# Kernel optimization log

Hardware: AMD Instinct MI355X
Metric: run time of the kernel (lower is better)

The kernel has to match this reference:

```python
import jax, jax.numpy as jnp
import numpy as np

M, N, P, T = 8000, 63, 64, 5


def setup_inputs() -> dict:
    key = jax.random.key(0)
    ks = jax.random.split(key, 19)
    sn = (1.0 / N) ** 0.5
    sp = (1.0 / P) ** 0.5
    f32 = jnp.float32
    return {
        "A": jax.random.normal(ks[0], (1, M, N), f32),
        "b": jax.random.normal(ks[1], (1, M), f32),
        "c": jax.random.normal(ks[2], (1, N), f32),
        "theta1r": sn * jax.random.normal(ks[3], (P, N + 1), f32),
        "theta1c": sn * jax.random.normal(ks[4], (P, N + 1), f32),
        "theta2rr": sp * jax.random.normal(ks[5], (P, P), f32),
        "theta2rc": sp * jax.random.normal(ks[6], (P, P), f32),
        "theta2cr": sp * jax.random.normal(ks[7], (P, P), f32),
        "theta3rr": sp * jax.random.normal(ks[8], (P, P), f32),
        "theta3rc": sp * jax.random.normal(ks[9], (P, P), f32),
        "theta3cr": sp * jax.random.normal(ks[10], (P, P), f32),
        "theta4rr": sp * jax.random.normal(ks[11], (P,), f32),
        "theta4rc": sp * jax.random.normal(ks[12], (P,), f32),
        "theta4cr": sp * jax.random.normal(ks[13], (P,), f32),
        "theta6r": sp * jax.random.normal(ks[14], (P, P), f32),
        "theta6c": sp * jax.random.normal(ks[15], (P, P), f32),
        "theta7": sp * jax.random.normal(ks[16], (P, P), f32),
        "W8": 0.05 * jax.random.normal(ks[17], (2, 2 * P), f32),
        "b8": 0.05 * jax.random.normal(ks[18], (2,), f32),
        "z": 7,
    }


def reference(A, b, c, theta1r, theta1c, theta2rr, theta2rc, theta2cr,
              theta3rr, theta3rc, theta3cr, theta4rr, theta4rc, theta4cr,
              theta6r, theta6c, theta7, W8, b8, z):
    relu = jax.nn.relu
    m, n = A.shape[1], A.shape[2]
    p = theta1r.shape[0]
    # raw node features: row node v -> [A[v,:], b[v]]; column node m -> [c, 0]
    Fr_raw = jnp.concatenate([A[0], b[0][:, None]], axis=1)        # (m, n+1)
    fc_raw = jnp.concatenate([c[0], jnp.zeros((1,), A.dtype)])     # (n+1,)
    Fr = Fr_raw / jnp.linalg.norm(Fr_raw, axis=1, keepdims=True)   # f(v), v < m
    fc = fc_raw / jnp.linalg.norm(fc_raw)                          # f(m)
    # edge weights w(v,u) = f(v).f(u) are detached in the original (float(...data))
    Frd = jax.lax.stop_gradient(Fr)
    fcd = jax.lax.stop_gradient(fc)
    Wrr = Frd @ Frd.T                                              # (m, m)
    dg = jnp.diagonal(Wrr)
    srr_pos = relu(Wrr).sum(axis=1) - relu(dg)                     # sum over u != v
    srr_neg = relu(-Wrr).sum(axis=1) - relu(-dg)
    wrc = Frd @ fcd                                                # (m,) = w(v, m)
    # identity: sum_u relu(t4 * w_u) = relu(t4) * sum_u relu(w_u) + relu(-t4) * sum_u relu(-w_u)
    Srr = relu(theta4rr)[:, None] * srr_pos[None, :] + relu(-theta4rr)[:, None] * srr_neg[None, :]
    Src = relu(theta4rc)[:, None] * relu(wrc)[None, :] + relu(-theta4rc)[:, None] * relu(-wrc)[None, :]
    scr = relu(theta4cr) * relu(wrc).sum() + relu(-theta4cr) * relu(-wrc).sum()
    edge_r = theta3rr @ Srr + theta3rc @ Src                       # (p, m), constant over t
    edge_c = theta3cr @ scr                                        # (p,)
    fz = Fr[z]                                                     # z < m: row node feature
    t1r = theta1r @ fz                                             # (p,)
    t1c = theta1c @ fz
    # mu init (p, m+1) = [[Ab^T, c0^T]; 0]; split into row columns / column node
    mu_r0 = jnp.zeros((p, m), A.dtype).at[: n + 1].set(Fr_raw.T)
    mu_c0 = jnp.zeros((p,), A.dtype).at[: n + 1].set(fc_raw)

    def step(carry, _):
        mu_r, mu_c = carry
        # row nodes: term2rr uses old mu[:, v]; term2rc uses old mu[:, m]
        new_r = relu(t1r[:, None] + theta2rr @ mu_r + (theta2rc @ mu_c)[:, None] + edge_r)
        # column node updated last within a sweep -> sees updated row embeddings
        new_c = relu(t1c + theta2cr @ new_r.sum(axis=1) + edge_c)
        return (new_r, new_c), None

    (mu_r, mu_c), _ = jax.lax.scan(step, (mu_r0, mu_c0), None, length=T)
    term6 = theta6r @ mu_r.sum(axis=1) + theta6c @ mu_c            # (p,)
    term7 = theta7 @ mu_r[:, z]                                    # (p,)
    feat = jax.nn.sigmoid(jnp.concatenate([term6, term7]))         # (2p,)
    return (feat @ W8.T + b8)[None, :]                             # (1, 2)
```

## Files before the change

kernel.cpp:

```cpp
#include <hip/hip_runtime.h>
#include <math.h>

typedef __attribute__((ext_vector_type(8))) short short8;
typedef __attribute__((ext_vector_type(4))) float f32x4;

#define WS_SPART 0
#define WS_GPART 131072
#define WS_WPART 163840
#define WS_CPART 164864
#define WS_T1R   204864
#define WS_T1C   204928
#define WS_AL    204992
#define WS_BE    205056
#define WS_GA    205120
#define WS_DE    205184
#define WS_ECP   205248
#define WS_ECN   205312
#define WS_W     205376
#define WS_MUZ   205760
#define WS_WSUM  205824
#define WS_RNORM 205888
#define WS_R2H   214080
#define WS_R2L   216128
#define WS_E4    218176
#define WS_FH    250176
#define WS_FL    512320

__device__ __forceinline__ float waveReduceSum(float v) {
#pragma unroll
    for (int m = 32; m >= 1; m >>= 1) v += __shfl_xor(v, m, 64);
    return v;
}
__device__ __forceinline__ unsigned short f2bf(float f) {
    unsigned int u = __float_as_uint(f);
    unsigned int r = (u + 0x7fffu + ((u >> 16) & 1u)) >> 16;
    return (unsigned short)r;
}
__device__ __forceinline__ float bf2f(unsigned short h) {
    return __uint_as_float(((unsigned int)h) << 16);
}

__global__ __launch_bounds__(256) void k_fr(
    const float* __restrict__ A, const float* __restrict__ b, const float* __restrict__ c,
    const float* __restrict__ th1r, const float* __restrict__ th1c,
    const float* __restrict__ th2rr, const float* __restrict__ th2rc,
    const float* __restrict__ th3rr, const float* __restrict__ th3rc, const float* __restrict__ th3cr,
    const float* __restrict__ th4rr, const float* __restrict__ th4rc, const float* __restrict__ th4cr,
    const int* __restrict__ zp,
    unsigned short* __restrict__ Fh, unsigned short* __restrict__ Fl,
    unsigned short* __restrict__ R2H, unsigned short* __restrict__ R2L,
    float* __restrict__ ws)
{
    int tid = threadIdx.x, lane = tid & 63, wid = tid >> 6;

    if (blockIdx.x == 512) {
        __shared__ float fcraw[64], fz[64], sh4a[64], sh4b[64];
        int p = lane;
        int z = zp[0];
        float cv = (p < 63) ? c[p] : 0.f;
        fcraw[p] = cv;
        float av = (p < 63) ? A[z * 63 + p] : b[z];
        float s2 = waveReduceSum(av * av);
        fz[p] = av * rsqrtf(s2);
        __syncthreads();

        float t1 = 0.f, t2 = 0.f, w0 = 0.f;
#pragma unroll 8
        for (int k = 0; k < 64; k++) {
            t1 += th1r[p * 64 + k] * fz[k];
            t2 += th1c[p * 64 + k] * fz[k];
            w0 += th2rc[p * 64 + k] * fcraw[k];
        }
        ws[WS_T1R + p] = t1;
        ws[WS_T1C + p] = t2;
        ws[WS_W + p] = t1 + w0;

        sh4a[p] = th4rr[p];
        sh4b[p] = th4rc[p];
        __syncthreads();
        float a = 0.f, bb = 0.f, g = 0.f, d = 0.f;
#pragma unroll 8
        for (int k = 0; k < 64; k++) {
            float t4 = sh4a[k];
            a  += th3rr[p * 64 + k] * fmaxf(t4, 0.f);
            bb += th3rr[p * 64 + k] * fmaxf(-t4, 0.f);
            float t5 = sh4b[k];
            g  += th3rc[p * 64 + k] * fmaxf(t5, 0.f);
            d  += th3rc[p * 64 + k] * fmaxf(-t5, 0.f);
        }
        ws[WS_AL + p] = a; ws[WS_BE + p] = bb;
        ws[WS_GA + p] = g; ws[WS_DE + p] = d;
        __syncthreads();
        sh4a[p] = th4cr[p];
        __syncthreads();
        float e1 = 0.f, e2 = 0.f;
#pragma unroll 8
        for (int k = 0; k < 64; k++) {
            float t6 = sh4a[k];
            e1 += th3cr[p * 64 + k] * fmaxf(t6, 0.f);
            e2 += th3cr[p * 64 + k] * fmaxf(-t6, 0.f);
        }
        ws[WS_ECP + p] = e1; ws[WS_ECN + p] = e2;

#pragma unroll
        for (int i = 0; i < 16; i++) {
            int idx = tid * 16 + i;
            float f = th2rr[idx];
            unsigned short h = f2bf(f);
            R2H[idx] = h;
            R2L[idx] = f2bf(f - bf2f(h));
        }
        return;
    }

    __shared__ float gsh[64];
    __shared__ float wsh2[2];
    if (tid < 64) gsh[tid] = 0.f;
    if (tid < 2) wsh2[tid] = 0.f;
    __syncthreads();

    float cv = (lane < 63) ? c[lane] : 0.f;
    float cn2 = waveReduceSum(cv * cv);
    float fcnl = cv * rsqrtf(cn2);

    int r0 = blockIdx.x * 16 + wid * 4;
    float gl = 0.f, lp = 0.f, ln = 0.f;
#pragma unroll
    for (int i = 0; i < 4; i++) {
        int r = r0 + i;
        if (r < 8000) {
            float val = (lane < 63) ? A[r * 63 + lane] : b[r];
            float s2 = waveReduceSum(val * val);
            float f = val * rsqrtf(s2);
            unsigned short h = f2bf(f);
            Fh[r * 64 + lane] = h;
            Fl[r * 64 + lane] = f2bf(f - bf2f(h));
            gl += f;
            float w = waveReduceSum(f * fcnl);
            if (lane == 0) {
                ws[WS_RNORM + r] = sqrtf(s2);
                lp += fmaxf(w, 0.f); ln += fmaxf(-w, 0.f);
            }
        } else {
            Fh[r * 64 + lane] = 0;
            Fl[r * 64 + lane] = 0;
        }
    }
    atomicAdd(&gsh[lane], gl);
    if (lane == 0) { atomicAdd(&wsh2[0], lp); atomicAdd(&wsh2[1], ln); }
    __syncthreads();
    if (tid < 64) ws[WS_GPART + blockIdx.x * 64 + tid] = gsh[tid];
    if (tid == 64) ws[WS_WPART + blockIdx.x * 2 + 0] = wsh2[0];
    if (tid == 65) ws[WS_WPART + blockIdx.x * 2 + 1] = wsh2[1];
}

__global__ __launch_bounds__(256) void k_gram(
    const unsigned short* __restrict__ Fh, float* __restrict__ ws)
{
    __shared__ short Bsh[2][32 * 72];
    int tid = threadIdx.x, lane = tid & 63, wid = tid >> 6;
    int m = lane & 15, quad = lane >> 4;
    int vbase = blockIdx.x * 256 + wid * 64;
    int srow = tid >> 3;
    int scol = (tid & 7) * 8;

    short8 AH[8];
#pragma unroll
    for (int pt = 0; pt < 4; pt++)
#pragma unroll
        for (int q = 0; q < 2; q++)
            AH[pt * 2 + q] = *(const short8*)(Fh + (vbase + pt * 16 + m) * 64 + q * 32 + quad * 8);

    float srr[16];
#pragma unroll
    for (int i = 0; i < 16; i++) srr[i] = 0.f;

    const int y = blockIdx.y;
    *(short8*)(&Bsh[0][srow * 72 + scol]) = *(const short8*)(Fh + (y * 32 + srow) * 64 + scol);
    __syncthreads();

#pragma unroll 1
    for (int k = 0; k < 16; k++) {
        int cur = k & 1;
        short8 pre;
        if (k < 15) {
            int cch = y + 16 * (k + 1);
            pre = *(const short8*)(Fh + (cch * 32 + srow) * 64 + scol);
        }
#pragma unroll
        for (int s = 0; s < 2; s++) {
            short8 BH[2];
#pragma unroll
            for (int q = 0; q < 2; q++)
                BH[q] = *(const short8*)(&Bsh[cur][(s * 16 + m) * 72 + q * 32 + quad * 8]);
#pragma unroll
            for (int pt = 0; pt < 4; pt++) {
                f32x4 a = {0.f, 0.f, 0.f, 0.f};
                a = __builtin_amdgcn_mfma_f32_16x16x32_bf16(AH[pt * 2 + 0], BH[0], a, 0, 0, 0);
                a = __builtin_amdgcn_mfma_f32_16x16x32_bf16(AH[pt * 2 + 1], BH[1], a, 0, 0, 0);
#pragma unroll
                for (int r = 0; r < 4; r++) srr[pt * 4 + r] += fmaxf(a[r], 0.f);
            }
        }
        if (k < 15) {
            *(short8*)(&Bsh[1 - cur][srow * 72 + scol]) = pre;
            __syncthreads();
        }
    }
#pragma unroll
    for (int pt = 0; pt < 4; pt++)
#pragma unroll
        for (int r = 0; r < 4; r++) {
            float s = srr[pt * 4 + r];
            s += __shfl_xor(s, 1, 64); s += __shfl_xor(s, 2, 64);
            s += __shfl_xor(s, 4, 64); s += __shfl_xor(s, 8, 64);
            if (m == 0)
                ws[WS_SPART + y * 8192 + vbase + pt * 16 + quad * 4 + r] = s;
        }
}

__global__ __launch_bounds__(256) void k_mu0(
    const float* __restrict__ c, float* __restrict__ ws,
    unsigned short* __restrict__ MH, unsigned short* __restrict__ ML,
    const unsigned short* __restrict__ R2H, const unsigned short* __restrict__ R2L)
{
    __shared__ float XF[64][68];
    __shared__ float red[256], colp[256];
    __shared__ __align__(16) float wS[64], alS[64], beS[64], gaS[64], deS[64];
    __shared__ float fcnS[64], gS[64], sprow[64];
    __shared__ __align__(16) float e4sh[256];
    int tid = threadIdx.x, lane = tid & 63, wid = tid >> 6;
    int m = lane & 15, quad = lane >> 4;
    int v0 = blockIdx.x * 64;
    int cw = wid * 16 + m;
    int v = v0 + cw;

    if (wid == 0) {
        float cv = (lane < 63) ? c[lane] : 0.f;
        float cn2 = waveReduceSum(cv * cv);
        fcnS[lane] = cv * rsqrtf(cn2);
        wS[lane] = ws[WS_W + lane];
    } else if (wid == 1) {
        alS[lane] = ws[WS_AL + lane]; beS[lane] = ws[WS_BE + lane];
        float wp = 0.f;
#pragma unroll
        for (int k = 0; k < 8; k++) wp += ws[WS_WPART + (lane + 64 * k) * 2];
        wp = waveReduceSum(wp);
        if (lane == 0) ws[WS_WSUM] = wp;
    } else if (wid == 2) {
        gaS[lane] = ws[WS_GA + lane]; deS[lane] = ws[WS_DE + lane];
        float wn = 0.f;
#pragma unroll
        for (int k = 0; k < 8; k++) wn += ws[WS_WPART + (lane + 64 * k) * 2 + 1];
        wn = waveReduceSum(wn);
        if (lane == 0) ws[WS_WSUM + 1] = wn;
    }
    float gv = 0.f;
#pragma unroll 8
    for (int bb = 0; bb < 128; bb++) gv += ws[WS_GPART + (wid * 128 + bb) * 64 + lane];
    red[tid] = gv;
    __syncthreads();
    if (tid < 64) gS[tid] = red[tid] + red[64 + tid] + red[128 + tid] + red[192 + tid];
    __syncthreads();
    float sv = 0.f;
#pragma unroll
    for (int y = wid * 4; y < wid * 4 + 4; y++) sv += ws[WS_SPART + y * 8192 + v0 + lane];
    red[tid] = sv;
    __syncthreads();
    if (tid < 64) sprow[tid] = red[tid] + red[64 + tid] + red[128 + tid] + red[192 + tid];
    __syncthreads();

    for (int i2 = 0; i2 < 16; i2++) {
        int i = wid * 16 + i2;
        int vr = v0 + i;
        float fr = bf2f(MH[vr * 64 + lane]) + bf2f(ML[vr * 64 + lane]);
        float dw = waveReduceSum(fr * fcnS[lane]);
        float dg = waveReduceSum(fr * gS[lane]);
        if (lane == 0) {
            float spv = sprow[i];
            float4 e;
            e.x = spv - 1.0f;
            e.y = spv - dg;
            e.z = fmaxf(dw, 0.f);
            e.w = fmaxf(-dw, 0.f);
            *(float4*)(&e4sh[i * 4]) = e;
            *(float4*)(ws + WS_E4 + vr * 4) = e;
        }
        XF[i][lane] = fr * ws[WS_RNORM + vr];
    }

    short8 RH[8], RL[8];
#pragma unroll
    for (int pt = 0; pt < 4; pt++)
#pragma unroll
        for (int q = 0; q < 2; q++) {
            int off = (pt * 16 + m) * 64 + q * 32 + quad * 8;
            RH[pt * 2 + q] = *(const short8*)(R2H + off);
            RL[pt * 2 + q] = *(const short8*)(R2L + off);
        }
    __syncthreads();

    short8 BH[2], BL[2];
#pragma unroll
    for (int q = 0; q < 2; q++) {
        float4 f0 = *(const float4*)(&XF[cw][q * 32 + quad * 8]);
        float4 f1 = *(const float4*)(&XF[cw][q * 32 + quad * 8 + 4]);
        float xv[8] = {f0.x, f0.y, f0.z, f0.w, f1.x, f1.y, f1.z, f1.w};
        short8 H, L;
#pragma unroll
        for (int j = 0; j < 8; j++) {
            unsigned short h = f2bf(xv[j]);
            H[j] = (short)h;
            L[j] = (short)f2bf(xv[j] - bf2f(h));
        }
        BH[q] = H; BL[q] = L;
    }
    float4 e = *(const float4*)(&e4sh[cw * 4]);

#pragma unroll
    for (int pt = 0; pt < 4; pt++) {
        f32x4 a = {0.f, 0.f, 0.f, 0.f};
#pragma unroll
        for (int q = 0; q < 2; q++) {
            a = __builtin_amdgcn_mfma_f32_16x16x32_bf16(RH[pt*2+q], BH[q], a, 0, 0, 0);
            a = __builtin_amdgcn_mfma_f32_16x16x32_bf16(RH[pt*2+q], BL[q], a, 0, 0, 0);
            a = __builtin_amdgcn_mfma_f32_16x16x32_bf16(RL[pt*2+q], BH[q], a, 0, 0, 0);
        }
        int pbase = pt * 16 + quad * 4;
        float4 w4 = *(const float4*)(wS + pbase);
        float4 a4 = *(const float4*)(alS + pbase);
        float4 b4 = *(const float4*)(beS + pbase);
        float4 g4 = *(const float4*)(gaS + pbase);
        float4 d4 = *(const float4*)(deS + pbase);
        float u0 = fmaxf(a[0] + w4.x + a4.x*e.x + b4.x*e.y + g4.x*e.z + d4.x*e.w, 0.f);
        float u1 = fmaxf(a[1] + w4.y + a4.y*e.x + b4.y*e.y + g4.y*e.z + d4.y*e.w, 0.f);
        float u2 = fmaxf(a[2] + w4.z + a4.z*e.x + b4.z*e.y + g4.z*e.z + d4.z*e.w, 0.f);
        float u3 = fmaxf(a[3] + w4.w + a4.w*e.x + b4.w*e.y + g4.w*e.z + d4.w*e.w, 0.f);
        ushort4 h4, l4;
        h4.x = f2bf(u0); l4.x = f2bf(u0 - bf2f(h4.x));
        h4.y = f2bf(u1); l4.y = f2bf(u1 - bf2f(h4.y));
        h4.z = f2bf(u2); l4.z = f2bf(u2 - bf2f(h4.z));
        h4.w = f2bf(u3); l4.w = f2bf(u3 - bf2f(h4.w));
        *(ushort4*)(MH + v * 64 + pbase) = h4;
        *(ushort4*)(ML + v * 64 + pbase) = l4;
        float c0 = u0, c1 = u1, c2 = u2, c3 = u3;
#pragma unroll
        for (int mm = 1; mm < 16; mm <<= 1) {
            c0 += __shfl_xor(c0, mm, 64);
            c1 += __shfl_xor(c1, mm, 64);
            c2 += __shfl_xor(c2, mm, 64);
            c3 += __shfl_xor(c3, mm, 64);
        }
        if (m == 0) {
            colp[wid * 64 + pbase + 0] = c0;
            colp[wid * 64 + pbase + 1] = c1;
            colp[wid * 64 + pbase + 2] = c2;
            colp[wid * 64 + pbase + 3] = c3;
        }
    }
    __syncthreads();
    if (tid < 64)
        ws[WS_CPART + blockIdx.x * 64 + tid] =
            colp[tid] + colp[64 + tid] + colp[128 + tid] + colp[192 + tid];
}

__global__ __launch_bounds__(256) void k_mu(
    const int* __restrict__ zp, float* __restrict__ ws,
    unsigned short* __restrict__ MH, unsigned short* __restrict__ ML,
    const unsigned short* __restrict__ R2H, const unsigned short* __restrict__ R2L,
    int t)
{
    __shared__ __align__(16) float wS[64], alS[64], beS[64], gaS[64], deS[64];
    __shared__ float colp[256];
    int tid = threadIdx.x, lane = tid & 63, wid = tid >> 6;
    int m = lane & 15, quad = lane >> 4;
    int v = (blockIdx.x * 4 + wid) * 16 + m;
    int z = zp[0];

    if (wid == 0) wS[lane] = ws[WS_W + t * 64 + lane];
    else if (wid == 1) { alS[lane] = ws[WS_AL + lane]; beS[lane] = ws[WS_BE + lane]; }
    else if (wid == 2) { gaS[lane] = ws[WS_GA + lane]; deS[lane] = ws[WS_DE + lane]; }

    short8 RH[8], RL[8];
#pragma unroll
    for (int pt = 0; pt < 4; pt++)
#pragma unroll
        for (int q = 0; q < 2; q++) {
            int off = (pt * 16 + m) * 64 + q * 32 + quad * 8;
            RH[pt * 2 + q] = *(const short8*)(R2H + off);
            RL[pt * 2 + q] = *(const short8*)(R2L + off);
        }
    short8 BH[2], BL[2];
#pragma unroll
    for (int q = 0; q < 2; q++) {
        BH[q] = *(const short8*)(MH + v * 64 + q * 32 + quad * 8);
        BL[q] = *(const short8*)(ML + v * 64 + q * 32 + quad * 8);
    }
    float4 e = *(const float4*)(ws + WS_E4 + v * 4);
    __syncthreads();

#pragma unroll
    for (int pt = 0; pt < 4; pt++) {
        f32x4 a = {0.f, 0.f, 0.f, 0.f};
#pragma unroll
        for (int q = 0; q < 2; q++) {
            a = __builtin_amdgcn_mfma_f32_16x16x32_bf16(RH[pt*2+q], BH[q], a, 0, 0, 0);
            a = __builtin_amdgcn_mfma_f32_16x16x32_bf16(RH[pt*2+q], BL[q], a, 0, 0, 0);
            a = __builtin_amdgcn_mfma_f32_16x16x32_bf16(RL[pt*2+q], BH[q], a, 0, 0, 0);
        }
        int pbase = pt * 16 + quad * 4;
        float4 w4 = *(const float4*)(wS + pbase);
        float4 a4 = *(const float4*)(alS + pbase);
        float4 b4 = *(const float4*)(beS + pbase);
        float4 g4 = *(const float4*)(gaS + pbase);
        float4 d4 = *(const float4*)(deS + pbase);
        float u0 = fmaxf(a[0] + w4.x + a4.x*e.x + b4.x*e.y + g4.x*e.z + d4.x*e.w, 0.f);
        float u1 = fmaxf(a[1] + w4.y + a4.y*e.x + b4.y*e.y + g4.y*e.z + d4.y*e.w, 0.f);
        float u2 = fmaxf(a[2] + w4.z + a4.z*e.x + b4.z*e.y + g4.z*e.z + d4.z*e.w, 0.f);
        float u3 = fmaxf(a[3] + w4.w + a4.w*e.x + b4.w*e.y + g4.w*e.z + d4.w*e.w, 0.f);
        ushort4 h4, l4;
        h4.x = f2bf(u0); l4.x = f2bf(u0 - bf2f(h4.x));
        h4.y = f2bf(u1); l4.y = f2bf(u1 - bf2f(h4.y));
        h4.z = f2bf(u2); l4.z = f2bf(u2 - bf2f(h4.z));
        h4.w = f2bf(u3); l4.w = f2bf(u3 - bf2f(h4.w));
        *(ushort4*)(MH + v * 64 + pbase) = h4;
        *(ushort4*)(ML + v * 64 + pbase) = l4;
        float c0 = u0, c1 = u1, c2 = u2, c3 = u3;
#pragma unroll
        for (int mm = 1; mm < 16; mm <<= 1) {
            c0 += __shfl_xor(c0, mm, 64);
            c1 += __shfl_xor(c1, mm, 64);
            c2 += __shfl_xor(c2, mm, 64);
            c3 += __shfl_xor(c3, mm, 64);
        }
        if (m == 0) {
            colp[wid * 64 + pbase + 0] = c0;
            colp[wid * 64 + pbase + 1] = c1;
            colp[wid * 64 + pbase + 2] = c2;
            colp[wid * 64 + pbase + 3] = c3;
        }
        if (t == 4 && v == z) {
            float4 o; o.x = u0; o.y = u1; o.z = u2; o.w = u3;
            *(float4*)(ws + WS_MUZ + pbase) = o;
        }
    }
    __syncthreads();
    if (tid < 64)
        ws[WS_CPART + t * 8000 + blockIdx.x * 64 + tid] =
            colp[tid] + colp[64 + tid] + colp[128 + tid] + colp[192 + tid];
}

__global__ __launch_bounds__(256) void k_colup(
    const float* __restrict__ th2cr, const float* __restrict__ th2rc,
    const float* __restrict__ th6r, const float* __restrict__ th6c,
    const float* __restrict__ th7, const float* __restrict__ W8,
    const float* __restrict__ b8,
    float* __restrict__ ws, float* __restrict__ out, int t)
{
    __shared__ float red[256], Ssh[64], ysh[64], wsh[64], feat[128];
    int tid = threadIdx.x, lane = tid & 63, wid = tid >> 6;
    int m = lane & 15, quad = lane >> 4;

    float s = 0.f;
    for (int blk = wid; blk < 125; blk += 4)
        s += ws[WS_CPART + t * 8000 + blk * 64 + lane];
    red[tid] = s;
    __syncthreads();
    if (tid < 64) Ssh[tid] = red[tid] + red[64 + tid] + red[128 + tid] + red[192 + tid];
    __syncthreads();
    {
        int p = wid * 16 + m;
        float acc = 0.f;
        const float4* rowp = (const float4*)(th2cr + p * 64 + quad * 16);
#pragma unroll
        for (int kk = 0; kk < 4; kk++) {
            float4 r4 = rowp[kk];
            acc += r4.x * Ssh[quad * 16 + 4 * kk]     + r4.y * Ssh[quad * 16 + 4 * kk + 1]
                 + r4.z * Ssh[quad * 16 + 4 * kk + 2] + r4.w * Ssh[quad * 16 + 4 * kk + 3];
        }
        acc += __shfl_xor(acc, 16, 64);
        acc += __shfl_xor(acc, 32, 64);
        if (quad == 0)
            ysh[p] = fmaxf(acc + ws[WS_T1C + p] + ws[WS_WSUM] * ws[WS_ECP + p]
                           + ws[WS_WSUM + 1] * ws[WS_ECN + p], 0.f);
    }
    __syncthreads();
    {
        int p = wid * 16 + m;
        float acc = 0.f;
        const float4* rowp = (const float4*)(th2rc + p * 64 + quad * 16);
#pragma unroll
        for (int kk = 0; kk < 4; kk++) {
            float4 r4 = rowp[kk];
            acc += r4.x * ysh[quad * 16 + 4 * kk]     + r4.y * ysh[quad * 16 + 4 * kk + 1]
                 + r4.z * ysh[quad * 16 + 4 * kk + 2] + r4.w * ysh[quad * 16 + 4 * kk + 3];
        }
        acc += __shfl_xor(acc, 16, 64);
        acc += __shfl_xor(acc, 32, 64);
        if (quad == 0) wsh[p] = acc + ws[WS_T1R + p];
    }
    __syncthreads();
    if (tid < 64) ws[WS_W + (t + 1) * 64 + tid] = wsh[tid];

    if (t == 4) {
        int p = tid;
        if (p < 64) {
            float t6 = 0.f, t7 = 0.f;
#pragma unroll 8
            for (int k = 0; k < 64; k++) {
                t6 += th6r[p * 64 + k] * Ssh[k] + th6c[p * 64 + k] * ysh[k];
                t7 += th7[p * 64 + k] * ws[WS_MUZ + k];
            }
            feat[p] = 1.f / (1.f + expf(-t6));
            feat[64 + p] = 1.f / (1.f + expf(-t7));
        }
        __syncthreads();
        if (p < 2) {
            float o = b8[p];
            for (int i = 0; i < 128; i++) o += W8[p * 128 + i] * feat[i];
            out[p] = o;
        }
    }
}

extern "C" void kernel_launch(void* const* d_in, const int* in_sizes, int n_in,
                              void* d_out, int out_size, void* d_ws, size_t ws_size,
                              hipStream_t stream) {
    (void)in_sizes; (void)n_in; (void)out_size; (void)ws_size;
    const float* A     = (const float*)d_in[0];
    const float* b     = (const float*)d_in[1];
    const float* c     = (const float*)d_in[2];
    const float* th1r  = (const float*)d_in[3];
    const float* th1c  = (const float*)d_in[4];
    const float* th2rr = (const float*)d_in[5];
    const float* th2rc = (const float*)d_in[6];
    const float* th2cr = (const float*)d_in[7];
    const float* th3rr = (const float*)d_in[8];
    const float* th3rc = (const float*)d_in[9];
    const float* th3cr = (const float*)d_in[10];
    const float* th4rr = (const float*)d_in[11];
    const float* th4rc = (const float*)d_in[12];
    const float* th4cr = (const float*)d_in[13];
    const float* th6r  = (const float*)d_in[14];
    const float* th6c  = (const float*)d_in[15];
    const float* th7   = (const float*)d_in[16];
    const float* W8    = (const float*)d_in[17];
    const float* b8    = (const float*)d_in[18];
    const int*   zp    = (const int*)d_in[19];
    float* ws  = (float*)d_ws;
    float* out = (float*)d_out;
    unsigned short* Fh  = (unsigned short*)(ws + WS_FH);
    unsigned short* Fl  = (unsigned short*)(ws + WS_FL);
    unsigned short* R2H = (unsigned short*)(ws + WS_R2H);
    unsigned short* R2L = (unsigned short*)(ws + WS_R2L);

    k_fr<<<513, 256, 0, stream>>>(A, b, c, th1r, th1c, th2rr, th2rc, th3rr, th3rc,
                                  th3cr, th4rr, th4rc, th4cr, zp, Fh, Fl, R2H, R2L, ws);
    k_gram<<<dim3(32, 16), 256, 0, stream>>>(Fh, ws);
    k_mu0<<<125, 256, 0, stream>>>(c, ws, Fh, Fl, R2H, R2L);
    for (int t = 0; t < 5; t++) {
        k_colup<<<1, 256, 0, stream>>>(th2cr, th2rc, th6r, th6c, th7, W8, b8, ws, out, t);
        if (t < 4)
            k_mu<<<125, 256, 0, stream>>>(zp, ws, Fh, Fl, R2H, R2L, t + 1);
    }
}
```

Measured before the change: 224.3 us.

## Fuse column-node update into k_mu and drop LDS staging in gram kernel

The single-block k_colup launches between iterations are removed. Every k_mu block now reduces the column partials itself and recomputes the column-node update and the row bias, and a separate k_head kernel computes the final output. This removes four serial one-block launches at the cost of redundant small matvecs in each of the 125 blocks. The gram kernel also stops staging B tiles in LDS and loads 16-row tiles straight into registers with a two-stage register prefetch. Its grid is doubled in y, so the partial-sum workspace and its reduction grow to match.

Result: no change. 223.9 us (-0.2%).

```diff
diff --git a/kernel.cpp b/kernel.cpp
--- a/kernel.cpp
+++ b/kernel.cpp
@@ -5,26 +5,26 @@
 typedef __attribute__((ext_vector_type(4))) float f32x4;
 
 #define WS_SPART 0
-#define WS_GPART 131072
-#define WS_WPART 163840
-#define WS_CPART 164864
-#define WS_T1R   204864
-#define WS_T1C   204928
-#define WS_AL    204992
-#define WS_BE    205056
-#define WS_GA    205120
-#define WS_DE    205184
-#define WS_ECP   205248
-#define WS_ECN   205312
-#define WS_W     205376
-#define WS_MUZ   205760
-#define WS_WSUM  205824
-#define WS_RNORM 205888
-#define WS_R2H   214080
-#define WS_R2L   216128
-#define WS_E4    218176
-#define WS_FH    250176
-#define WS_FL    512320
+#define WS_GPART 262144
+#define WS_WPART 294912
+#define WS_CPART 295936
+#define WS_T1R   335936
+#define WS_T1C   336000
+#define WS_AL    336064
+#define WS_BE    336128
+#define WS_GA    336192
+#define WS_DE    336256
+#define WS_ECP   336320
+#define WS_ECN   336384
+#define WS_W     336448
+#define WS_MUZ   336512
+#define WS_WSUM  336576
+#define WS_RNORM 336640
+#define WS_R2H   344832
+#define WS_R2L   346880
+#define WS_E4    348928
+#define WS_FH    380928
+#define WS_FL    643072
 
 __device__ __forceinline__ float waveReduceSum(float v) {
 #pragma unroll
@@ -157,12 +157,9 @@
 __global__ __launch_bounds__(256) void k_gram(
     const unsigned short* __restrict__ Fh, float* __restrict__ ws)
 {
-    __shared__ short Bsh[2][32 * 72];
     int tid = threadIdx.x, lane = tid & 63, wid = tid >> 6;
     int m = lane & 15, quad = lane >> 4;
     int vbase = blockIdx.x * 256 + wid * 64;
-    int srow = tid >> 3;
-    int scol = (tid & 7) * 8;
 
     short8 AH[8];
 #pragma unroll
@@ -176,35 +173,39 @@
     for (int i = 0; i < 16; i++) srr[i] = 0.f;
 
     const int y = blockIdx.y;
-    *(short8*)(&Bsh[0][srow * 72 + scol]) = *(const short8*)(Fh + (y * 32 + srow) * 64 + scol);
-    __syncthreads();
+    const int boff = m * 64 + quad * 8;
+    short8 B0[2], B1[2];
+#pragma unroll
+    for (int q = 0; q < 2; q++)
+        B0[q] = *(const short8*)(Fh + y * 16 * 64 + boff + q * 32);
 
 #pragma unroll 1
-    for (int k = 0; k < 16; k++) {
-        int cur = k & 1;
-        short8 pre;
-        if (k < 15) {
-            int cch = y + 16 * (k + 1);
-            pre = *(const short8*)(Fh + (cch * 32 + srow) * 64 + scol);
-        }
-#pragma unroll
-        for (int s = 0; s < 2; s++) {
-            short8 BH[2];
+    for (int k2 = 0; k2 < 8; k2++) {
+        int jB1 = y + 32 * (2 * k2 + 1);
+#pragma unroll
+        for (int q = 0; q < 2; q++)
+            B1[q] = *(const short8*)(Fh + jB1 * 16 * 64 + boff + q * 32);
+#pragma unroll
+        for (int pt = 0; pt < 4; pt++) {
+            f32x4 a = {0.f, 0.f, 0.f, 0.f};
+            a = __builtin_amdgcn_mfma_f32_16x16x32_bf16(AH[pt * 2 + 0], B0[0], a, 0, 0, 0);
+            a = __builtin_amdgcn_mfma_f32_16x16x32_bf16(AH[pt * 2 + 1], B0[1], a, 0, 0, 0);
+#pragma unroll
+            for (int r = 0; r < 4; r++) srr[pt * 4 + r] += fmaxf(a[r], 0.f);
+        }
+        if (k2 < 7) {
+            int jB0 = y + 32 * (2 * k2 + 2);
 #pragma unroll
             for (int q = 0; q < 2; q++)
-                BH[q] = *(const short8*)(&Bsh[cur][(s * 16 + m) * 72 + q * 32 + quad * 8]);
-#pragma unroll
-            for (int pt = 0; pt < 4; pt++) {
-                f32x4 a = {0.f, 0.f, 0.f, 0.f};
-                a = __builtin_amdgcn_mfma_f32_16x16x32_bf16(AH[pt * 2 + 0], BH[0], a, 0, 0, 0);
-                a = __builtin_amdgcn_mfma_f32_16x16x32_bf16(AH[pt * 2 + 1], BH[1], a, 0, 0, 0);
-#pragma unroll
-                for (int r = 0; r < 4; r++) srr[pt * 4 + r] += fmaxf(a[r], 0.f);
-            }
-        }
-        if (k < 15) {
-            *(short8*)(&Bsh[1 - cur][srow * 72 + scol]) = pre;
-            __syncthreads();
+                B0[q] = *(const short8*)(Fh + jB0 * 16 * 64 + boff + q * 32);
+        }
+#pragma unroll
+        for (int pt = 0; pt < 4; pt++) {
+            f32x4 a = {0.f, 0.f, 0.f, 0.f};
+            a = __builtin_amdgcn_mfma_f32_16x16x32_bf16(AH[pt * 2 + 0], B1[0], a, 0, 0, 0);
+            a = __builtin_amdgcn_mfma_f32_16x16x32_bf16(AH[pt * 2 + 1], B1[1], a, 0, 0, 0);
+#pragma unroll
+            for (int r = 0; r < 4; r++) srr[pt * 4 + r] += fmaxf(a[r], 0.f);
         }
     }
 #pragma unroll
@@ -264,7 +265,7 @@
     __syncthreads();
     float sv = 0.f;
 #pragma unroll
-    for (int y = wid * 4; y < wid * 4 + 4; y++) sv += ws[WS_SPART + y * 8192 + v0 + lane];
+    for (int y = wid * 8; y < wid * 8 + 8; y++) sv += ws[WS_SPART + y * 8192 + v0 + lane];
     red[tid] = sv;
     __syncthreads();
     if (tid < 64) sprow[tid] = red[tid] + red[64 + tid] + red[128 + tid] + red[192 + tid];
@@ -365,21 +366,62 @@
 }
 
 __global__ __launch_bounds__(256) void k_mu(
+    const float* __restrict__ th2cr, const float* __restrict__ th2rc,
     const int* __restrict__ zp, float* __restrict__ ws,
     unsigned short* __restrict__ MH, unsigned short* __restrict__ ML,
     const unsigned short* __restrict__ R2H, const unsigned short* __restrict__ R2L,
     int t)
 {
+    __shared__ float red[256], colp[256];
     __shared__ __align__(16) float wS[64], alS[64], beS[64], gaS[64], deS[64];
-    __shared__ float colp[256];
+    __shared__ float Ssh[64], ysh[64];
     int tid = threadIdx.x, lane = tid & 63, wid = tid >> 6;
     int m = lane & 15, quad = lane >> 4;
     int v = (blockIdx.x * 4 + wid) * 16 + m;
     int z = zp[0];
 
-    if (wid == 0) wS[lane] = ws[WS_W + t * 64 + lane];
-    else if (wid == 1) { alS[lane] = ws[WS_AL + lane]; beS[lane] = ws[WS_BE + lane]; }
-    else if (wid == 2) { gaS[lane] = ws[WS_GA + lane]; deS[lane] = ws[WS_DE + lane]; }
+    if (tid < 64) {
+        alS[tid] = ws[WS_AL + tid]; beS[tid] = ws[WS_BE + tid];
+        gaS[tid] = ws[WS_GA + tid]; deS[tid] = ws[WS_DE + tid];
+    }
+    float s = 0.f;
+    for (int blk = wid; blk < 125; blk += 4)
+        s += ws[WS_CPART + (t - 1) * 8000 + blk * 64 + lane];
+    red[tid] = s;
+    __syncthreads();
+    if (tid < 64) Ssh[tid] = red[tid] + red[64 + tid] + red[128 + tid] + red[192 + tid];
+    __syncthreads();
+    {
+        int p = wid * 16 + m;
+        float acc = 0.f;
+        const float4* rowp = (const float4*)(th2cr + p * 64 + quad * 16);
+#pragma unroll
+        for (int kk = 0; kk < 4; kk++) {
+            float4 r4 = rowp[kk];
+            acc += r4.x * Ssh[quad * 16 + 4 * kk]     + r4.y * Ssh[quad * 16 + 4 * kk + 1]
+                 + r4.z * Ssh[quad * 16 + 4 * kk + 2] + r4.w * Ssh[quad * 16 + 4 * kk + 3];
+        }
+        acc += __shfl_xor(acc, 16, 64);
+        acc += __shfl_xor(acc, 32, 64);
+        if (quad == 0)
+            ysh[p] = fmaxf(acc + ws[WS_T1C + p] + ws[WS_WSUM] * ws[WS_ECP + p]
+                           + ws[WS_WSUM + 1] * ws[WS_ECN + p], 0.f);
+    }
+    __syncthreads();
+    {
+        int p = wid * 16 + m;
+        float acc = 0.f;
+        const float4* rowp = (const float4*)(th2rc + p * 64 + quad * 16);
+#pragma unroll
+        for (int kk = 0; kk < 4; kk++) {
+            float4 r4 = rowp[kk];
+            acc += r4.x * ysh[quad * 16 + 4 * kk]     + r4.y * ysh[quad * 16 + 4 * kk + 1]
+                 + r4.z * ysh[quad * 16 + 4 * kk + 2] + r4.w * ysh[quad * 16 + 4 * kk + 3];
+        }
+        acc += __shfl_xor(acc, 16, 64);
+        acc += __shfl_xor(acc, 32, 64);
+        if (quad == 0) wS[p] = acc + ws[WS_T1R + p];
+    }
 
     short8 RH[8], RL[8];
 #pragma unroll
@@ -450,76 +492,47 @@
             colp[tid] + colp[64 + tid] + colp[128 + tid] + colp[192 + tid];
 }
 
-__global__ __launch_bounds__(256) void k_colup(
-    const float* __restrict__ th2cr, const float* __restrict__ th2rc,
+__global__ __launch_bounds__(256) void k_head(
+    const float* __restrict__ th2cr,
     const float* __restrict__ th6r, const float* __restrict__ th6c,
     const float* __restrict__ th7, const float* __restrict__ W8,
     const float* __restrict__ b8,
-    float* __restrict__ ws, float* __restrict__ out, int t)
+    float* __restrict__ ws, float* __restrict__ out)
 {
-    __shared__ float red[256], Ssh[64], ysh[64], wsh[64], feat[128];
+    __shared__ float red[256], Ssh[64], ysh[64], feat[128];
     int tid = threadIdx.x, lane = tid & 63, wid = tid >> 6;
-    int m = lane & 15, quad = lane >> 4;
 
     float s = 0.f;
     for (int blk = wid; blk < 125; blk += 4)
-        s += ws[WS_CPART + t * 8000 + blk * 64 + lane];
+        s += ws[WS_CPART + 4 * 8000 + blk * 64 + lane];
     red[tid] = s;
     __syncthreads();
     if (tid < 64) Ssh[tid] = red[tid] + red[64 + tid] + red[128 + tid] + red[192 + tid];
     __syncthreads();
-    {
-        int p = wid * 16 + m;
-        float acc = 0.f;
-        const float4* rowp = (const float4*)(th2cr + p * 64 + quad * 16);
-#pragma unroll
-        for (int kk = 0; kk < 4; kk++) {
-            float4 r4 = rowp[kk];
-            acc += r4.x * Ssh[quad * 16 + 4 * kk]     + r4.y * Ssh[quad * 16 + 4 * kk + 1]
-                 + r4.z * Ssh[quad * 16 + 4 * kk + 2] + r4.w * Ssh[quad * 16 + 4 * kk + 3];
-        }
-        acc += __shfl_xor(acc, 16, 64);
-        acc += __shfl_xor(acc, 32, 64);
-        if (quad == 0)
-            ysh[p] = fmaxf(acc + ws[WS_T1C + p] + ws[WS_WSUM] * ws[WS_ECP + p]
-                           + ws[WS_WSUM + 1] * ws[WS_ECN + p], 0.f);
-    }
-    __syncthreads();
-    {
-        int p = wid * 16 + m;
-        float acc = 0.f;
-        const float4* rowp = (const float4*)(th2rc + p * 64 + quad * 16);
-#pragma unroll
-        for (int kk = 0; kk < 4; kk++) {
-            float4 r4 = rowp[kk];
-            acc += r4.x * ysh[quad * 16 + 4 * kk]     + r4.y * ysh[quad * 16 + 4 * kk + 1]
-                 + r4.z * ysh[quad * 16 + 4 * kk + 2] + r4.w * ysh[quad * 16 + 4 * kk + 3];
-        }
-        acc += __shfl_xor(acc, 16, 64);
-        acc += __shfl_xor(acc, 32, 64);
-        if (quad == 0) wsh[p] = acc + ws[WS_T1R + p];
-    }
-    __syncthreads();
-    if (tid < 64) ws[WS_W + (t + 1) * 64 + tid] = wsh[tid];
-
-    if (t == 4) {
-        int p = tid;
-        if (p < 64) {
-            float t6 = 0.f, t7 = 0.f;
+    int p = tid;
+    if (p < 64) {
+        float acc = ws[WS_T1C + p] + ws[WS_WSUM] * ws[WS_ECP + p]
+                  + ws[WS_WSUM + 1] * ws[WS_ECN + p];
 #pragma unroll 8
-            for (int k = 0; k < 64; k++) {
-                t6 += th6r[p * 64 + k] * Ssh[k] + th6c[p * 64 + k] * ysh[k];
-                t7 += th7[p * 64 + k] * ws[WS_MUZ + k];
-            }
-            feat[p] = 1.f / (1.f + expf(-t6));
-            feat[64 + p] = 1.f / (1.f + expf(-t7));
-        }
-        __syncthreads();
-        if (p < 2) {
-            float o = b8[p];
-            for (int i = 0; i < 128; i++) o += W8[p * 128 + i] * feat[i];
-            out[p] = o;
-        }
+        for (int k = 0; k < 64; k++) acc += th2cr[p * 64 + k] * Ssh[k];
+        ysh[p] = fmaxf(acc, 0.f);
+    }
+    __syncthreads();
+    if (p < 64) {
+        float t6 = 0.f, t7 = 0.f;
+#pragma unroll 8
+        for (int k = 0; k < 64; k++) {
+            t6 += th6r[p * 64 + k] * Ssh[k] + th6c[p * 64 + k] * ysh[k];
+            t7 += th7[p * 64 + k] * ws[WS_MUZ + k];
+        }
+        feat[p] = 1.f / (1.f + expf(-t6));
+        feat[64 + p] = 1.f / (1.f + expf(-t7));
+    }
+    __syncthreads();
+    if (p < 2) {
+        float o = b8[p];
+        for (int i = 0; i < 128; i++) o += W8[p * 128 + i] * feat[i];
+        out[p] = o;
     }
 }
 
@@ -556,11 +569,9 @@
 
     k_fr<<<513, 256, 0, stream>>>(A, b, c, th1r, th1c, th2rr, th2rc, th3rr, th3rc,
                                   th3cr, th4rr, th4rc, th4cr, zp, Fh, Fl, R2H, R2L, ws);
-    k_gram<<<dim3(32, 16), 256, 0, stream>>>(Fh, ws);
+    k_gram<<<dim3(32, 32), 256, 0, stream>>>(Fh, ws);
     k_mu0<<<125, 256, 0, stream>>>(c, ws, Fh, Fl, R2H, R2L);
-    for (int t = 0; t < 5; t++) {
-        k_colup<<<1, 256, 0, stream>>>(th2cr, th2rc, th6r, th6c, th7, W8, b8, ws, out, t);
-        if (t < 4)
-            k_mu<<<125, 256, 0, stream>>>(zp, ws, Fh, Fl, R2H, R2L, t + 1);
-    }
-}
+    for (int t = 1; t < 5; t++)
+        k_mu<<<125, 256, 0, stream>>>(th2cr, th2rc, zp, ws, Fh, Fl, R2H, R2L, t);
+    k_head<<<1, 256, 0, stream>>>(th2cr, th6r, th6c, th7, W8, b8, ws, out);
+}
```
